# Kernel tuning notes

Measured on AMD Instinct MI355X. Metric: run time of the kernel, lower is better.

The kernel has to match this reference:

```python
import jax, jax.numpy as jnp
import numpy as np

N_RAYS = 32768
HID = 64
MARCH_ITERS = 64
EPS = 1e-4
NEAR = 0.0
FAR = 1.0
T_FAR = 1.0
TPUT_B = 64
JITTER = 1.0 / TPUT_B  # fixed stand-in for random.random() * (2 / batch_size)


def _init_linear(key, fan_in, fan_out):
    kw, kb = jax.random.split(key)
    lim = 1.0 / np.sqrt(fan_in)
    W = jax.random.uniform(kw, (fan_in, fan_out), jnp.float32, -lim, lim)
    b = jax.random.uniform(kb, (fan_out,), jnp.float32, -lim, lim)
    return W, b


def setup_inputs() -> dict:
    key = jax.random.key(0)
    ks = jax.random.split(key, 6)
    rays = jax.random.normal(ks[0], (N_RAYS, 6), jnp.float32)
    W0, b0 = _init_linear(ks[1], 3, HID)
    W1, b1 = _init_linear(ks[2], HID, HID)
    W2, b2 = _init_linear(ks[3], HID, 1)
    Wr0, br0 = _init_linear(ks[4], 6, HID)
    Wr1, br1 = _init_linear(ks[5], HID, 3)
    return dict(rays=rays, W0=W0, b0=b0, W1=W1, b1=b1, W2=W2, b2=b2,
                Wr0=Wr0, br0=br0, Wr1=Wr1, br1=br1)


def _sdf(p, W0, b0, W1, b1, W2, b2):
    # p: [N, 3] -> signed distance [N, 1]
    h = jax.nn.relu(p @ W0 + b0)
    h = jax.nn.relu(h @ W1 + b1)
    return h @ W2 + b2


def _refl(p, d, Wr0, br0, Wr1, br1):
    # p, d: [N, 3] -> RGB [N, 3]
    h = jax.nn.relu(jnp.concatenate([p, d], axis=-1) @ Wr0 + br0)
    return jax.nn.sigmoid(h @ Wr1 + br1)


def reference(rays, W0, b0, W1, b1, W2, b2, Wr0, br0, Wr1, br1):
    r_o, r_d = rays[..., :3], rays[..., 3:]
    sdf = lambda p: _sdf(p, W0, b0, W1, b1, W2, b2)

    # --- sphere march (64 fixed iterations; early-exit break is a no-op
    # once all rays hit, since hit rays stop updating) ---
    hits0 = jnp.zeros(r_o.shape[:-1] + (1,), jnp.bool_)
    dist0 = jnp.full(r_o.shape[:-1] + (1,), NEAR, jnp.float32)

    def march(carry, _):
        hits, cd = carry
        d = sdf(r_o + r_d * cd)  # [N, 1]
        hits = hits | ((d < EPS) & (cd >= NEAR) & (cd <= FAR))
        cd = jnp.where(~hits, cd + d, cd)
        return (hits, cd), None

    (hit, t), _ = jax.lax.scan(march, (hits0, dist0), None, length=MARCH_ITERS)
    pts = r_o + r_d * t

    rgb = _refl(pts, r_d, Wr0, br0, Wr1, br1)
    rgb = jnp.where(hit, rgb, 0.0)  # out[~hit] = 0

    # --- throughput (index search under no_grad in the original) ---
    max_t = T_FAR + JITTER
    step = max_t / TPUT_B
    sg = jax.lax.stop_gradient
    sdf_ng = lambda p: _sdf(p, sg(W0), sg(b0), sg(W1), sg(b1), sg(W2), sg(b2))
    r_o_ng, r_d_ng = sg(r_o), sg(r_d)

    curr_min0 = sdf_ng(r_o_ng)[..., 0]          # [N]
    idxs0 = jnp.zeros_like(curr_min0, jnp.int32)

    def tloop(carry, i):
        cm, idxs = carry
        t_i = step * (i + 1).astype(jnp.float32)
        sd = sdf_ng(r_o_ng + t_i * r_d_ng)[..., 0]
        idxs = jnp.where(sd < cm, i + 1, idxs)
        return (jnp.minimum(cm, sd), idxs), None

    (_, idxs), _ = jax.lax.scan(tloop, (curr_min0, idxs0),
                                jnp.arange(TPUT_B, dtype=jnp.int32))

    best_pos = r_o + idxs[..., None].astype(jnp.float32) * step * r_d  # [N, 3]
    tput = sdf(best_pos)  # [N, 1], differentiable (outside no_grad in torch)

    return jnp.concatenate([rgb, tput], axis=-1)  # [N, 4]
```

## Files before the change

kernel.cpp:

```cpp
#include <hip/hip_runtime.h>
#include <math.h>

#define NRAYS        32768
#define MARCH_ITERS  64
#define EPS_         1e-4f
#define STEP_        ((1.0f + 1.0f/64.0f) / 64.0f)

typedef __attribute__((ext_vector_type(8)))  short    short8;
typedef __attribute__((ext_vector_type(4)))  float    float4v;
typedef __attribute__((ext_vector_type(4)))  unsigned uint4v;

__device__ __forceinline__ short8 mk_frag(unsigned p0, unsigned p1,
                                          unsigned p2, unsigned p3) {
    uint4v v = {p0, p1, p2, p3};
    return __builtin_bit_cast(short8, v);
}

__device__ __forceinline__ unsigned packbf(unsigned a, unsigned b) {
    return __builtin_amdgcn_perm(b, a, 0x07060302u);
}

struct Split3 { unsigned h, m, l; };
__device__ __forceinline__ Split3 split3(float x) {
    unsigned xu = __float_as_uint(x);
    float xh = __uint_as_float(xu & 0xFFFF0000u);
    float r  = x - xh;
    unsigned ru = __float_as_uint(r);
    float xm = __uint_as_float(ru & 0xFFFF0000u);
    float r2 = r - xm;
    return { xu, ru, __float_as_uint(r2) };
}

struct Split2 { unsigned h, r; };
__device__ __forceinline__ Split2 split2(float x) {
    unsigned xu = __float_as_uint(x);
    float xh = __uint_as_float(xu & 0xFFFF0000u);
    float rr = x - xh;
    return { xu, __float_as_uint(rr) };
}

__global__ __launch_bounds__(64)
__attribute__((amdgpu_waves_per_eu(2, 8)))
void sdf_w9_k(
    const float* __restrict__ rays,
    const float* __restrict__ W0,  const float* __restrict__ b0,
    const float* __restrict__ W1,  const float* __restrict__ b1,
    const float* __restrict__ W2,  const float* __restrict__ b2,
    const float* __restrict__ Wr0, const float* __restrict__ br0,
    const float* __restrict__ Wr1, const float* __restrict__ br1,
    float* __restrict__ out)
{
    const int lane = threadIdx.x;
    const int kind = blockIdx.x & 1;
    const int quad = lane >> 4;
    const int m    = lane & 15;
    const int rayBase = (blockIdx.x >> 1) * 16;

    const float* rp = rays + (rayBase + m) * 6;
    const float ox = rp[0], oy = rp[1], oz = rp[2];
    const float dx = rp[3], dy = rp[4], dz = rp[5];

    short8 A1[4];
    {
        const float* wbase = (quad == 0) ? W0 : (quad == 1) ? (W0 + 64)
                           : (quad == 2) ? (W0 + 128) : b0;
        #pragma unroll
        for (int t = 0; t < 4; ++t) {
            int j = 32 * (t >> 1) + 8 * (m >> 2) + 4 * (t & 1) + (m & 3);
            Split3 s = split3(wbase[j]);
            unsigned hh = packbf(s.h, s.h);
            unsigned hm = packbf(s.h, s.m);
            unsigned ml = packbf(s.m, s.l);
            unsigned l0 = packbf(s.l, 0u);
            bool is3 = (quad == 3);
            A1[t] = mk_frag(is3 ? hm : hh, is3 ? l0 : hm, is3 ? 0u : ml, 0u);
        }
    }

    float4v b1v[4], w2v[4];
    #pragma unroll
    for (int t = 0; t < 4; ++t) {
        int base = 16 * t + 4 * quad;
        b1v[t] = (float4v){b1[base], b1[base + 1], b1[base + 2], b1[base + 3]};
        w2v[t] = (float4v){W2[base], W2[base + 1], W2[base + 2], W2[base + 3]};
    }
    const float b2s = b2[0];
    const float4v z4 = {0.f, 0.f, 0.f, 0.f};

    auto buildB1 = [&](float px, float py, float pz) -> short8 {
        float c = (quad == 0) ? px : (quad == 1) ? py : pz;
        Split3 s = split3(c);
        unsigned d0 = packbf(s.h, s.m);
        unsigned d1 = packbf(s.l, s.h);
        unsigned d2 = packbf(s.m, s.h);
        if (quad == 3) { d0 = 0x3F803F80u; d1 = 0x00003F80u; d2 = 0u; }
        return mk_frag(d0, d1, d2, 0u);
    };

    auto front = [&](float px, float py, float pz, short8* BH, short8* BM) {
        short8 B1 = buildB1(px, py, pz);
        float4v C1[4];
        #pragma unroll
        for (int t = 0; t < 4; ++t)
            C1[t] = __builtin_amdgcn_mfma_f32_16x16x32_bf16(A1[t], B1, z4, 0, 0, 0);
        unsigned PH[4][2], PM[4][2];
        #pragma unroll
        for (int t = 0; t < 4; ++t) {
            float v0 = fmaxf(C1[t][0], 0.f), v1 = fmaxf(C1[t][1], 0.f);
            float v2 = fmaxf(C1[t][2], 0.f), v3 = fmaxf(C1[t][3], 0.f);
            unsigned u0 = __float_as_uint(v0), u1 = __float_as_uint(v1);
            unsigned u2 = __float_as_uint(v2), u3 = __float_as_uint(v3);
            PH[t][0] = packbf(u0, u1); PH[t][1] = packbf(u2, u3);
            float r0 = v0 - __uint_as_float(u0 & 0xFFFF0000u);
            float r1 = v1 - __uint_as_float(u1 & 0xFFFF0000u);
            float r2 = v2 - __uint_as_float(u2 & 0xFFFF0000u);
            float r3 = v3 - __uint_as_float(u3 & 0xFFFF0000u);
            PM[t][0] = packbf(__float_as_uint(r0), __float_as_uint(r1));
            PM[t][1] = packbf(__float_as_uint(r2), __float_as_uint(r3));
        }
        #pragma unroll
        for (int h = 0; h < 2; ++h) {
            BH[h] = mk_frag(PH[2 * h][0], PH[2 * h][1],
                            PH[2 * h + 1][0], PH[2 * h + 1][1]);
            BM[h] = mk_frag(PM[2 * h][0], PM[2 * h][1],
                            PM[2 * h + 1][0], PM[2 * h + 1][1]);
        }
    };

    auto l3 = [&](const float4v* C2) -> float {
        float q0 = 0.f, q1 = 0.f, q2 = 0.f, q3 = 0.f;
        #pragma unroll
        for (int t = 0; t < 4; ++t) {
            q0 = fmaf(fmaxf(C2[t][0], 0.f), w2v[t][0], q0);
            q1 = fmaf(fmaxf(C2[t][1], 0.f), w2v[t][1], q1);
            q2 = fmaf(fmaxf(C2[t][2], 0.f), w2v[t][2], q2);
            q3 = fmaf(fmaxf(C2[t][3], 0.f), w2v[t][3], q3);
        }
        float part = (q0 + q1) + (q2 + q3);
        part += __shfl_xor(part, 16, 64);
        part += __shfl_xor(part, 32, 64);
        return b2s + part;
    };

    if (kind == 0) {
        short8 A2h[2][4], A2m[2][4];
        #pragma unroll
        for (int h = 0; h < 2; ++h)
            #pragma unroll
            for (int t = 0; t < 4; ++t) {
                unsigned pm[4], ph[4];
                #pragma unroll
                for (int jp = 0; jp < 4; ++jp) {
                    int k0 = 32 * h + quad * 8 + 2 * jp;
                    int j2 = 16 * t + m;
                    Split2 a = split2(W1[k0 * 64 + j2]);
                    Split2 b = split2(W1[(k0 + 1) * 64 + j2]);
                    pm[jp] = packbf(a.r, b.r);
                    ph[jp] = packbf(a.h, b.h);
                }
                A2m[h][t] = mk_frag(pm[0], pm[1], pm[2], pm[3]);
                A2h[h][t] = mk_frag(ph[0], ph[1], ph[2], ph[3]);
            }

        bool  hit = false;
        float cd  = 0.f;
        #pragma unroll 1
        for (int it = 0; it < MARCH_ITERS; ++it) {
            if (__all(hit)) break;
            short8 BH[2], BM[2];
            front(fmaf(dx, cd, ox), fmaf(dy, cd, oy), fmaf(dz, cd, oz), BH, BM);
            float4v C2[4];
            #pragma unroll
            for (int t = 0; t < 4; ++t) C2[t] = b1v[t];
            #pragma unroll
            for (int h = 0; h < 2; ++h)
                #pragma unroll
                for (int t = 0; t < 4; ++t)
                    C2[t] = __builtin_amdgcn_mfma_f32_16x16x32_bf16(
                        A2m[h][t], BH[h], C2[t], 0, 0, 0);
            #pragma unroll
            for (int h = 0; h < 2; ++h)
                #pragma unroll
                for (int t = 0; t < 4; ++t)
                    C2[t] = __builtin_amdgcn_mfma_f32_16x16x32_bf16(
                        A2h[h][t], BM[h], C2[t], 0, 0, 0);
            #pragma unroll
            for (int h = 0; h < 2; ++h)
                #pragma unroll
                for (int t = 0; t < 4; ++t)
                    C2[t] = __builtin_amdgcn_mfma_f32_16x16x32_bf16(
                        A2h[h][t], BH[h], C2[t], 0, 0, 0);
            float dm = l3(C2);
            bool c = (dm < EPS_) && (cd >= 0.f) && (cd <= 1.f);
            hit = hit || c;
            if (!hit) cd += dm;
        }

        const float px = fmaf(dx, cd, ox), py = fmaf(dy, cd, oy), pz = fmaf(dz, cd, oz);
        float r0 = 0.f, r1 = 0.f, r2 = 0.f;
        #pragma unroll 4
        for (int jj = 0; jj < 16; ++jj) {
            int j = quad * 16 + jj;
            float a = fmaf(px, Wr0[j],
                      fmaf(py, Wr0[64 + j],
                      fmaf(pz, Wr0[128 + j],
                      fmaf(dx, Wr0[192 + j],
                      fmaf(dy, Wr0[256 + j],
                      fmaf(dz, Wr0[320 + j], br0[j]))))));
            a = fmaxf(a, 0.f);
            r0 = fmaf(a, Wr1[j * 3 + 0], r0);
            r1 = fmaf(a, Wr1[j * 3 + 1], r1);
            r2 = fmaf(a, Wr1[j * 3 + 2], r2);
        }
        r0 += __shfl_xor(r0, 16, 64); r0 += __shfl_xor(r0, 32, 64);
        r1 += __shfl_xor(r1, 16, 64); r1 += __shfl_xor(r1, 32, 64);
        r2 += __shfl_xor(r2, 16, 64); r2 += __shfl_xor(r2, 32, 64);
        r0 = 1.f / (1.f + expf(-(r0 + br1[0])));
        r1 = 1.f / (1.f + expf(-(r1 + br1[1])));
        r2 = 1.f / (1.f + expf(-(r2 + br1[2])));
        if (!hit) { r0 = 0.f; r1 = 0.f; r2 = 0.f; }
        if (lane < 16) {
            float* op = out + (rayBase + lane) * 4;
            op[0] = r0; op[1] = r1; op[2] = r2;
        }
    } else {
        short8 A2h[2][4];
        #pragma unroll
        for (int h = 0; h < 2; ++h)
            #pragma unroll
            for (int t = 0; t < 4; ++t) {
                unsigned ph[4];
                #pragma unroll
                for (int jp = 0; jp < 4; ++jp) {
                    int k0 = 32 * h + quad * 8 + 2 * jp;
                    int j2 = 16 * t + m;
                    ph[jp] = packbf(__float_as_uint(W1[k0 * 64 + j2]),
                                    __float_as_uint(W1[(k0 + 1) * 64 + j2]));
                }
                A2h[h][t] = mk_frag(ph[0], ph[1], ph[2], ph[3]);
            }

        float cm = 3.4e38f;
        #pragma unroll 1
        for (int i = 0; i <= 64; ++i) {
            float ti = STEP_ * (float)i;
            short8 BH[2], BM[2];
            front(fmaf(dx, ti, ox), fmaf(dy, ti, oy), fmaf(dz, ti, oz), BH, BM);
            float4v C2[4];
            #pragma unroll
            for (int t = 0; t < 4; ++t) C2[t] = b1v[t];
            #pragma unroll
            for (int h = 0; h < 2; ++h)
                #pragma unroll
                for (int t = 0; t < 4; ++t)
                    C2[t] = __builtin_amdgcn_mfma_f32_16x16x32_bf16(
                        A2h[h][t], BM[h], C2[t], 0, 0, 0);
            #pragma unroll
            for (int h = 0; h < 2; ++h)
                #pragma unroll
                for (int t = 0; t < 4; ++t)
                    C2[t] = __builtin_amdgcn_mfma_f32_16x16x32_bf16(
                        A2h[h][t], BH[h], C2[t], 0, 0, 0);
            float dt = l3(C2);
            cm = fminf(cm, dt);
        }
        if (lane < 16)
            out[(rayBase + lane) * 4 + 3] = cm;
    }
}

extern "C" void kernel_launch(void* const* d_in, const int* in_sizes, int n_in,
                              void* d_out, int out_size, void* d_ws, size_t ws_size,
                              hipStream_t stream) {
    const float* rays = (const float*)d_in[0];
    const float* W0   = (const float*)d_in[1];
    const float* b0   = (const float*)d_in[2];
    const float* W1   = (const float*)d_in[3];
    const float* b1   = (const float*)d_in[4];
    const float* W2   = (const float*)d_in[5];
    const float* b2   = (const float*)d_in[6];
    const float* Wr0  = (const float*)d_in[7];
    const float* br0  = (const float*)d_in[8];
    const float* Wr1  = (const float*)d_in[9];
    const float* br1  = (const float*)d_in[10];
    float* out = (float*)d_out;

    hipLaunchKernelGGL(sdf_w9_k, dim3((NRAYS / 16) * 2), dim3(64), 0, stream,
                       rays, W0, b0, W1, b1, W2, b2, Wr0, br0, Wr1, br1, out);
}
```

Baseline: 181.8 us.

## Precompute per-ray affine first layer and evaluate it with packed FMAs instead of MFMA

The first SDF layer is linear in the march distance, so the per-ray terms o·W0+b0 and d·W0 are computed once and each iteration's layer-1 preactivation becomes one fused multiply-add per hidden unit. This removes four bf16-split MFMAs plus the three-way splitting of the point coordinates on every iteration. The hidden-unit math and the final dot product are written as two-wide float vectors so the compiler can emit packed FP32 instructions. Layer-1 values are now plain fp32 rather than the split-bf16 emulation, which slightly changes rounding.

After: 182.4 us. Within noise of the previous version (+0.4%).

```diff
diff --git a/kernel.cpp b/kernel.cpp
--- a/kernel.cpp
+++ b/kernel.cpp
@@ -8,6 +8,7 @@
 
 typedef __attribute__((ext_vector_type(8)))  short    short8;
 typedef __attribute__((ext_vector_type(4)))  float    float4v;
+typedef __attribute__((ext_vector_type(2)))  float    float2v;
 typedef __attribute__((ext_vector_type(4)))  unsigned uint4v;
 
 __device__ __forceinline__ short8 mk_frag(unsigned p0, unsigned p1,
@@ -18,17 +19,6 @@
 
 __device__ __forceinline__ unsigned packbf(unsigned a, unsigned b) {
     return __builtin_amdgcn_perm(b, a, 0x07060302u);
-}
-
-struct Split3 { unsigned h, m, l; };
-__device__ __forceinline__ Split3 split3(float x) {
-    unsigned xu = __float_as_uint(x);
-    float xh = __uint_as_float(xu & 0xFFFF0000u);
-    float r  = x - xh;
-    unsigned ru = __float_as_uint(r);
-    float xm = __uint_as_float(ru & 0xFFFF0000u);
-    float r2 = r - xm;
-    return { xu, ru, __float_as_uint(r2) };
 }
 
 struct Split2 { unsigned h, r; };
@@ -39,9 +29,13 @@
     return { xu, __float_as_uint(rr) };
 }
 
+__device__ __forceinline__ float2v fma2(float2v a, float2v b, float2v c) {
+    return __builtin_elementwise_fma(a, b, c);
+}
+
 __global__ __launch_bounds__(64)
 __attribute__((amdgpu_waves_per_eu(2, 8)))
-void sdf_w9_k(
+void sdf_w10_k(
     const float* __restrict__ rays,
     const float* __restrict__ W0,  const float* __restrict__ b0,
     const float* __restrict__ W1,  const float* __restrict__ b1,
@@ -60,63 +54,54 @@
     const float ox = rp[0], oy = rp[1], oz = rp[2];
     const float dx = rp[3], dy = rp[4], dz = rp[5];
 
-    short8 A1[4];
-    {
-        const float* wbase = (quad == 0) ? W0 : (quad == 1) ? (W0 + 64)
-                           : (quad == 2) ? (W0 + 128) : b0;
-        #pragma unroll
-        for (int t = 0; t < 4; ++t) {
-            int j = 32 * (t >> 1) + 8 * (m >> 2) + 4 * (t & 1) + (m & 3);
-            Split3 s = split3(wbase[j]);
-            unsigned hh = packbf(s.h, s.h);
-            unsigned hm = packbf(s.h, s.m);
-            unsigned ml = packbf(s.m, s.l);
-            unsigned l0 = packbf(s.l, 0u);
-            bool is3 = (quad == 3);
-            A1[t] = mk_frag(is3 ? hm : hh, is3 ? l0 : hm, is3 ? 0u : ml, 0u);
-        }
-    }
-
-    float4v b1v[4], w2v[4];
+    float2v a2[4][2], s2[4][2];
+    #pragma unroll
+    for (int t = 0; t < 4; ++t)
+        #pragma unroll
+        for (int p = 0; p < 2; ++p) {
+            float av[2], sv[2];
+            #pragma unroll
+            for (int e = 0; e < 2; ++e) {
+                int j = 32 * (t >> 1) + 8 * quad + 4 * (t & 1) + (2 * p + e);
+                float w0c = W0[j], w1c = W0[64 + j], w2c = W0[128 + j];
+                av[e] = fmaf(ox, w0c, fmaf(oy, w1c, fmaf(oz, w2c, b0[j])));
+                sv[e] = fmaf(dx, w0c, fmaf(dy, w1c, dz * w2c));
+            }
+            a2[t][p] = (float2v){av[0], av[1]};
+            s2[t][p] = (float2v){sv[0], sv[1]};
+        }
+
+    float4v b1v[4];
+    float2v w2a[4], w2b[4];
     #pragma unroll
     for (int t = 0; t < 4; ++t) {
         int base = 16 * t + 4 * quad;
         b1v[t] = (float4v){b1[base], b1[base + 1], b1[base + 2], b1[base + 3]};
-        w2v[t] = (float4v){W2[base], W2[base + 1], W2[base + 2], W2[base + 3]};
+        w2a[t] = (float2v){W2[base], W2[base + 1]};
+        w2b[t] = (float2v){W2[base + 2], W2[base + 3]};
     }
     const float b2s = b2[0];
-    const float4v z4 = {0.f, 0.f, 0.f, 0.f};
-
-    auto buildB1 = [&](float px, float py, float pz) -> short8 {
-        float c = (quad == 0) ? px : (quad == 1) ? py : pz;
-        Split3 s = split3(c);
-        unsigned d0 = packbf(s.h, s.m);
-        unsigned d1 = packbf(s.l, s.h);
-        unsigned d2 = packbf(s.m, s.h);
-        if (quad == 3) { d0 = 0x3F803F80u; d1 = 0x00003F80u; d2 = 0u; }
-        return mk_frag(d0, d1, d2, 0u);
-    };
-
-    auto front = [&](float px, float py, float pz, short8* BH, short8* BM) {
-        short8 B1 = buildB1(px, py, pz);
-        float4v C1[4];
-        #pragma unroll
-        for (int t = 0; t < 4; ++t)
-            C1[t] = __builtin_amdgcn_mfma_f32_16x16x32_bf16(A1[t], B1, z4, 0, 0, 0);
+
+    auto front = [&](float cv, short8* BH, short8* BM) {
+        const float2v c2 = {cv, cv};
         unsigned PH[4][2], PM[4][2];
         #pragma unroll
         for (int t = 0; t < 4; ++t) {
-            float v0 = fmaxf(C1[t][0], 0.f), v1 = fmaxf(C1[t][1], 0.f);
-            float v2 = fmaxf(C1[t][2], 0.f), v3 = fmaxf(C1[t][3], 0.f);
+            float2v v01 = fma2(c2, s2[t][0], a2[t][0]);
+            float2v v23 = fma2(c2, s2[t][1], a2[t][1]);
+            float v0 = fmaxf(v01.x, 0.f), v1 = fmaxf(v01.y, 0.f);
+            float v2 = fmaxf(v23.x, 0.f), v3 = fmaxf(v23.y, 0.f);
             unsigned u0 = __float_as_uint(v0), u1 = __float_as_uint(v1);
             unsigned u2 = __float_as_uint(v2), u3 = __float_as_uint(v3);
             PH[t][0] = packbf(u0, u1); PH[t][1] = packbf(u2, u3);
-            float r0 = v0 - __uint_as_float(u0 & 0xFFFF0000u);
-            float r1 = v1 - __uint_as_float(u1 & 0xFFFF0000u);
-            float r2 = v2 - __uint_as_float(u2 & 0xFFFF0000u);
-            float r3 = v3 - __uint_as_float(u3 & 0xFFFF0000u);
-            PM[t][0] = packbf(__float_as_uint(r0), __float_as_uint(r1));
-            PM[t][1] = packbf(__float_as_uint(r2), __float_as_uint(r3));
+            float2v h01 = {__uint_as_float(u0 & 0xFFFF0000u),
+                           __uint_as_float(u1 & 0xFFFF0000u)};
+            float2v h23 = {__uint_as_float(u2 & 0xFFFF0000u),
+                           __uint_as_float(u3 & 0xFFFF0000u)};
+            float2v r01 = (float2v){v0, v1} - h01;
+            float2v r23 = (float2v){v2, v3} - h23;
+            PM[t][0] = packbf(__float_as_uint(r01.x), __float_as_uint(r01.y));
+            PM[t][1] = packbf(__float_as_uint(r23.x), __float_as_uint(r23.y));
         }
         #pragma unroll
         for (int h = 0; h < 2; ++h) {
@@ -128,15 +113,15 @@
     };
 
     auto l3 = [&](const float4v* C2) -> float {
-        float q0 = 0.f, q1 = 0.f, q2 = 0.f, q3 = 0.f;
+        float2v q01 = {0.f, 0.f}, q23 = {0.f, 0.f};
         #pragma unroll
         for (int t = 0; t < 4; ++t) {
-            q0 = fmaf(fmaxf(C2[t][0], 0.f), w2v[t][0], q0);
-            q1 = fmaf(fmaxf(C2[t][1], 0.f), w2v[t][1], q1);
-            q2 = fmaf(fmaxf(C2[t][2], 0.f), w2v[t][2], q2);
-            q3 = fmaf(fmaxf(C2[t][3], 0.f), w2v[t][3], q3);
-        }
-        float part = (q0 + q1) + (q2 + q3);
+            float2v rel01 = {fmaxf(C2[t][0], 0.f), fmaxf(C2[t][1], 0.f)};
+            float2v rel23 = {fmaxf(C2[t][2], 0.f), fmaxf(C2[t][3], 0.f)};
+            q01 = fma2(rel01, w2a[t], q01);
+            q23 = fma2(rel23, w2b[t], q23);
+        }
+        float part = (q01.x + q01.y) + (q23.x + q23.y);
         part += __shfl_xor(part, 16, 64);
         part += __shfl_xor(part, 32, 64);
         return b2s + part;
@@ -168,16 +153,16 @@
         for (int it = 0; it < MARCH_ITERS; ++it) {
             if (__all(hit)) break;
             short8 BH[2], BM[2];
-            front(fmaf(dx, cd, ox), fmaf(dy, cd, oy), fmaf(dz, cd, oz), BH, BM);
+            front(cd, BH, BM);
             float4v C2[4];
             #pragma unroll
-            for (int t = 0; t < 4; ++t) C2[t] = b1v[t];
-            #pragma unroll
-            for (int h = 0; h < 2; ++h)
-                #pragma unroll
-                for (int t = 0; t < 4; ++t)
-                    C2[t] = __builtin_amdgcn_mfma_f32_16x16x32_bf16(
-                        A2m[h][t], BH[h], C2[t], 0, 0, 0);
+            for (int t = 0; t < 4; ++t)
+                C2[t] = __builtin_amdgcn_mfma_f32_16x16x32_bf16(
+                    A2m[0][t], BH[0], b1v[t], 0, 0, 0);
+            #pragma unroll
+            for (int t = 0; t < 4; ++t)
+                C2[t] = __builtin_amdgcn_mfma_f32_16x16x32_bf16(
+                    A2m[1][t], BH[1], C2[t], 0, 0, 0);
             #pragma unroll
             for (int h = 0; h < 2; ++h)
                 #pragma unroll
@@ -245,16 +230,16 @@
         for (int i = 0; i <= 64; ++i) {
             float ti = STEP_ * (float)i;
             short8 BH[2], BM[2];
-            front(fmaf(dx, ti, ox), fmaf(dy, ti, oy), fmaf(dz, ti, oz), BH, BM);
+            front(ti, BH, BM);
             float4v C2[4];
             #pragma unroll
-            for (int t = 0; t < 4; ++t) C2[t] = b1v[t];
-            #pragma unroll
-            for (int h = 0; h < 2; ++h)
-                #pragma unroll
-                for (int t = 0; t < 4; ++t)
-                    C2[t] = __builtin_amdgcn_mfma_f32_16x16x32_bf16(
-                        A2h[h][t], BM[h], C2[t], 0, 0, 0);
+            for (int t = 0; t < 4; ++t)
+                C2[t] = __builtin_amdgcn_mfma_f32_16x16x32_bf16(
+                    A2h[0][t], BM[0], b1v[t], 0, 0, 0);
+            #pragma unroll
+            for (int t = 0; t < 4; ++t)
+                C2[t] = __builtin_amdgcn_mfma_f32_16x16x32_bf16(
+                    A2h[1][t], BM[1], C2[t], 0, 0, 0);
             #pragma unroll
             for (int h = 0; h < 2; ++h)
                 #pragma unroll
@@ -285,6 +270,6 @@
     const float* br1  = (const float*)d_in[10];
     float* out = (float*)d_out;
 
-    hipLaunchKernelGGL(sdf_w9_k, dim3((NRAYS / 16) * 2), dim3(64), 0, stream,
+    hipLaunchKernelGGL(sdf_w10_k, dim3((NRAYS / 16) * 2), dim3(64), 0, stream,
                        rays, W0, b0, W1, b1, W2, b2, Wr0, br0, Wr1, br1, out);
 }
```
